# Performance work log

Hardware: AMD Instinct MI355X
Metric: run time of the kernel (lower is better)

Reference implementation:

```python
import jax, jax.numpy as jnp
import numpy as np

BATCH = 262144
CLUSTER = 100

def _boost_generators():
    # Standard Lorentz boost generators K_x, K_y, K_z (symmetric, metric (+,-,-,-)).
    K = np.zeros((3, 4, 4), dtype=np.float32)
    for j in range(3):
        K[j, 0, j + 1] = 1.0
        K[j, j + 1, 0] = 1.0
    return jnp.asarray(K)

def setup_inputs() -> dict:
    key = jax.random.key(0)
    k1, k2, k3, k4 = jax.random.split(key, 4)
    T = jax.random.normal(k1, (BATCH, CLUSTER, 4), dtype=jnp.float32)
    # build() initializes boosts/bias uniform[0,1) scaled by 0.33 (|b| < 1 => gamma real)
    Bo = jax.random.uniform(k2, (CLUSTER, 3), dtype=jnp.float32) * 0.33
    Bi = jax.random.uniform(k3, (1, 3), dtype=jnp.float32) * 0.33
    W = jax.random.uniform(k4, (CLUSTER, 1), dtype=jnp.float32)
    K_mats = _boost_generators()
    return {"T": T, "Bo": Bo, "Bi": Bi, "W": W, "K_mats": K_mats}

def _lorentz(x, boosts, K_mats, weights=None):
    # x: (batch, C, 4), boosts: (C, 3) -> (batch, 4)
    mag = jnp.sqrt(jnp.sum(boosts * boosts, axis=1, keepdims=True))  # (C,1)
    n = boosts / mag                                                  # (C,3)
    g = 1.0 / jnp.sqrt(1.0 - mag * mag)                               # (C,1) gamma
    nK = jnp.einsum('cj,jad->cad', n, K_mats)                         # (C,4,4)
    nK2 = jnp.einsum('cab,cbd->cad', nK, nK)                          # (C,4,4)
    B = (jnp.eye(4, dtype=x.dtype)[None]
         - (g * mag)[..., None] * nK
         + (g - 1.0)[..., None] * nK2)                                # (C,4,4)
    if weights is not None:
        B = weights[:, :, None] * B                                   # per-element scalar weight
    # sum over cluster of B_c @ x[:, c]
    return jnp.einsum('cad,bcd->ba', B, x)

def reference(T, Bo, Bi, W, K_mats):
    summed = _lorentz(T, Bo, K_mats, weights=W)            # (batch, 4)
    out = _lorentz(summed[:, None, :], Bi, K_mats)         # (batch, 4)
    return out.reshape(T.shape[0], 1, 4)
```

## Files before the change

### kernel.cpp

```cpp
#include <hip/hip_runtime.h>
#include <math.h>

#define BATCH   262144
#define CLUSTER 100

__device__ inline void boost_mat(float bx, float by, float bz, float B[4][4]) {
    float m2  = bx * bx + by * by + bz * bz;
    float mag = sqrtf(m2);
    float nx = bx / mag, ny = by / mag, nz = bz / mag;
    float g  = 1.0f / sqrtf(1.0f - mag * mag);
    float gm = g * mag;
    float gm1 = g - 1.0f;
    float n[3] = {nx, ny, nz};
    B[0][0] = 1.0f + gm1 * (nx * nx + ny * ny + nz * nz);
    for (int j = 0; j < 3; ++j) {
        B[0][j + 1] = -gm * n[j];
        B[j + 1][0] = -gm * n[j];
    }
    for (int i = 0; i < 3; ++i)
        for (int j = 0; j < 3; ++j)
            B[i + 1][j + 1] = ((i == j) ? 1.0f : 0.0f) + gm1 * n[i] * n[j];
}

#define DOT4(mm, vv) ((mm).x*(vv).x + (mm).y*(vv).y + (mm).z*(vv).z + (mm).w*(vv).w)

__global__ __launch_bounds__(256) void lorentz_fused_kernel(
        const float* __restrict__ T,
        const float* __restrict__ Bo,
        const float* __restrict__ Bi,
        const float* __restrict__ W,
        float* __restrict__ out) {
    __shared__ float sM[CLUSTER * 16];

    int tid = threadIdx.x;
    if (tid < CLUSTER) {
        float BiM[4][4], BoM[4][4];
        boost_mat(Bi[0], Bi[1], Bi[2], BiM);
        boost_mat(Bo[tid * 3 + 0], Bo[tid * 3 + 1], Bo[tid * 3 + 2], BoM);
        float w = W[tid];
        for (int a = 0; a < 4; ++a)
            for (int d = 0; d < 4; ++d) {
                float s = 0.0f;
                for (int e = 0; e < 4; ++e)
                    s += BiM[a][e] * (w * BoM[e][d]);
                sM[tid * 16 + a * 4 + d] = s;
            }
    }
    __syncthreads();

    int wave = tid >> 6;
    int lane = tid & 63;
    int q = lane & 7;
    int g = lane >> 3;
    long long base = (long long)blockIdx.x * 64 + wave * 16;
    long long row0 = base + g;
    long long row1 = base + g + 8;

    const float* P0 = T + row0 * (CLUSTER * 4);
    const float* P1 = T + row1 * (CLUSTER * 4);

    float4 a0 = {0.f, 0.f, 0.f, 0.f};
    float4 a1 = a0;

    #pragma unroll 4
    for (int t = 0; t < 12; ++t) {
        int c = 8 * t + q;
        float4 v0 = *(const float4*)(P0 + c * 4);
        float4 v1 = *(const float4*)(P1 + c * 4);
        const float4* m = (const float4*)(sM + c * 16);
        float4 m0 = m[0], m1 = m[1], m2 = m[2], m3 = m[3];
        a0.x += DOT4(m0, v0); a0.y += DOT4(m1, v0); a0.z += DOT4(m2, v0); a0.w += DOT4(m3, v0);
        a1.x += DOT4(m0, v1); a1.y += DOT4(m1, v1); a1.z += DOT4(m2, v1); a1.w += DOT4(m3, v1);
    }
    if (q < 4) {
        int c = 96 + q;
        float4 v0 = *(const float4*)(P0 + c * 4);
        float4 v1 = *(const float4*)(P1 + c * 4);
        const float4* m = (const float4*)(sM + c * 16);
        float4 m0 = m[0], m1 = m[1], m2 = m[2], m3 = m[3];
        a0.x += DOT4(m0, v0); a0.y += DOT4(m1, v0); a0.z += DOT4(m2, v0); a0.w += DOT4(m3, v0);
        a1.x += DOT4(m0, v1); a1.y += DOT4(m1, v1); a1.z += DOT4(m2, v1); a1.w += DOT4(m3, v1);
    }

    #define RED(f) f += __shfl_xor(f, 1); f += __shfl_xor(f, 2); f += __shfl_xor(f, 4);
    RED(a0.x) RED(a0.y) RED(a0.z) RED(a0.w)
    RED(a1.x) RED(a1.y) RED(a1.z) RED(a1.w)
    #undef RED

    if (q == 0) ((float4*)out)[row0] = a0;
    if (q == 1) ((float4*)out)[row1] = a1;
}

extern "C" void kernel_launch(void* const* d_in, const int* in_sizes, int n_in,
                              void* d_out, int out_size, void* d_ws, size_t ws_size,
                              hipStream_t stream) {
    const float* T  = (const float*)d_in[0];
    const float* Bo = (const float*)d_in[1];
    const float* Bi = (const float*)d_in[2];
    const float* W  = (const float*)d_in[3];

    float* out = (float*)d_out;

    int blocks = BATCH / 64;
    lorentz_fused_kernel<<<blocks, 256, 0, stream>>>(T, Bo, Bi, W, out);
}
```

Before: 77.82 us.

## Prefetch T before matrix setup and widen lane layout to four rows per thread

Issues the first global loads of T before the per-block boost-matrix computation and barrier, so memory latency overlaps the setup work. Each thread now handles four rows, with sixteen lanes per row instead of eight, and the next iteration's loads are software-pipelined. The shared matrix is stored in a row-split layout to change the LDS access pattern. This adds one extra shuffle stage in the reduction and uses more registers, which may reduce occupancy.

```diff
diff --git a/kernel.cpp b/kernel.cpp
--- a/kernel.cpp
+++ b/kernel.cpp
@@ -30,9 +30,25 @@
         const float* __restrict__ Bi,
         const float* __restrict__ W,
         float* __restrict__ out) {
-    __shared__ float sM[CLUSTER * 16];
+    __shared__ float sMr[4][CLUSTER * 4];
 
-    int tid = threadIdx.x;
+    int tid  = threadIdx.x;
+    int wave = tid >> 6;
+    int lane = tid & 63;
+    int q = lane & 15;
+    int g = lane >> 4;
+    long long base = (long long)blockIdx.x * 64 + wave * 16;
+
+    const float* P0 = T + (base + g +  0) * (CLUSTER * 4);
+    const float* P1 = T + (base + g +  4) * (CLUSTER * 4);
+    const float* P2 = T + (base + g +  8) * (CLUSTER * 4);
+    const float* P3 = T + (base + g + 12) * (CLUSTER * 4);
+
+    float4 v0 = *(const float4*)(P0 + q * 4);
+    float4 v1 = *(const float4*)(P1 + q * 4);
+    float4 v2 = *(const float4*)(P2 + q * 4);
+    float4 v3 = *(const float4*)(P3 + q * 4);
+
     if (tid < CLUSTER) {
         float BiM[4][4], BoM[4][4];
         boost_mat(Bi[0], Bi[1], Bi[2], BiM);
@@ -43,52 +59,62 @@
                 float s = 0.0f;
                 for (int e = 0; e < 4; ++e)
                     s += BiM[a][e] * (w * BoM[e][d]);
-                sM[tid * 16 + a * 4 + d] = s;
+                sMr[a][tid * 4 + d] = s;
             }
     }
     __syncthreads();
 
-    int wave = tid >> 6;
-    int lane = tid & 63;
-    int q = lane & 7;
-    int g = lane >> 3;
-    long long base = (long long)blockIdx.x * 64 + wave * 16;
-    long long row0 = base + g;
-    long long row1 = base + g + 8;
+    float4 a0 = {0.f, 0.f, 0.f, 0.f};
+    float4 a1 = a0, a2 = a0, a3 = a0;
 
-    const float* P0 = T + row0 * (CLUSTER * 4);
-    const float* P1 = T + row1 * (CLUSTER * 4);
+    #define ACCSTEP(c)                                                        \
+    {                                                                         \
+        float4 m0 = *(const float4*)&sMr[0][(c) * 4];                         \
+        float4 m1 = *(const float4*)&sMr[1][(c) * 4];                         \
+        float4 m2 = *(const float4*)&sMr[2][(c) * 4];                         \
+        float4 m3 = *(const float4*)&sMr[3][(c) * 4];                         \
+        a0.x += DOT4(m0, v0); a0.y += DOT4(m1, v0); a0.z += DOT4(m2, v0); a0.w += DOT4(m3, v0); \
+        a1.x += DOT4(m0, v1); a1.y += DOT4(m1, v1); a1.z += DOT4(m2, v1); a1.w += DOT4(m3, v1); \
+        a2.x += DOT4(m0, v2); a2.y += DOT4(m1, v2); a2.z += DOT4(m2, v2); a2.w += DOT4(m3, v2); \
+        a3.x += DOT4(m0, v3); a3.y += DOT4(m1, v3); a3.z += DOT4(m2, v3); a3.w += DOT4(m3, v3); \
+    }
 
-    float4 a0 = {0.f, 0.f, 0.f, 0.f};
-    float4 a1 = a0;
-
-    #pragma unroll 4
-    for (int t = 0; t < 12; ++t) {
-        int c = 8 * t + q;
-        float4 v0 = *(const float4*)(P0 + c * 4);
-        float4 v1 = *(const float4*)(P1 + c * 4);
-        const float4* m = (const float4*)(sM + c * 16);
-        float4 m0 = m[0], m1 = m[1], m2 = m[2], m3 = m[3];
-        a0.x += DOT4(m0, v0); a0.y += DOT4(m1, v0); a0.z += DOT4(m2, v0); a0.w += DOT4(m3, v0);
-        a1.x += DOT4(m0, v1); a1.y += DOT4(m1, v1); a1.z += DOT4(m2, v1); a1.w += DOT4(m3, v1);
+    for (int t = 0; t < 6; ++t) {
+        int c = 16 * t + q;
+        ACCSTEP(c)
+        if (t < 5) {
+            int cn = c + 16;
+            v0 = *(const float4*)(P0 + cn * 4);
+            v1 = *(const float4*)(P1 + cn * 4);
+            v2 = *(const float4*)(P2 + cn * 4);
+            v3 = *(const float4*)(P3 + cn * 4);
+        } else if (q < 4) {
+            int cn = 96 + q;
+            v0 = *(const float4*)(P0 + cn * 4);
+            v1 = *(const float4*)(P1 + cn * 4);
+            v2 = *(const float4*)(P2 + cn * 4);
+            v3 = *(const float4*)(P3 + cn * 4);
+        }
     }
     if (q < 4) {
-        int c = 96 + q;
-        float4 v0 = *(const float4*)(P0 + c * 4);
-        float4 v1 = *(const float4*)(P1 + c * 4);
-        const float4* m = (const float4*)(sM + c * 16);
-        float4 m0 = m[0], m1 = m[1], m2 = m[2], m3 = m[3];
-        a0.x += DOT4(m0, v0); a0.y += DOT4(m1, v0); a0.z += DOT4(m2, v0); a0.w += DOT4(m3, v0);
-        a1.x += DOT4(m0, v1); a1.y += DOT4(m1, v1); a1.z += DOT4(m2, v1); a1.w += DOT4(m3, v1);
+        ACCSTEP(96 + q)
     }
+    #undef ACCSTEP
 
-    #define RED(f) f += __shfl_xor(f, 1); f += __shfl_xor(f, 2); f += __shfl_xor(f, 4);
+    #define RED(f) f += __shfl_xor(f, 1); f += __shfl_xor(f, 2); \
+                   f += __shfl_xor(f, 4); f += __shfl_xor(f, 8);
     RED(a0.x) RED(a0.y) RED(a0.z) RED(a0.w)
     RED(a1.x) RED(a1.y) RED(a1.z) RED(a1.w)
+    RED(a2.x) RED(a2.y) RED(a2.z) RED(a2.w)
+    RED(a3.x) RED(a3.y) RED(a3.z) RED(a3.w)
     #undef RED
 
-    if (q == 0) ((float4*)out)[row0] = a0;
-    if (q == 1) ((float4*)out)[row1] = a1;
+    float4 o = a0;
+    if (q == 1) o = a1;
+    if (q == 2) o = a2;
+    if (q == 3) o = a3;
+    if (q < 4)
+        ((float4*)out)[base + g + 4 * q] = o;
 }
 
 extern "C" void kernel_launch(void* const* d_in, const int* in_sizes, int n_in,
```

New measurement: 82.90 us. 1.07x slower.

## Process multiple row tiles per block to amortize matrix setup

Applied to the files above, without the earlier changes.

Each block now loops over four 64-row tiles, so the per-block setup (computing the 100 combined boost matrices and the barrier) runs once per 256 rows instead of once per 64. The shared matrix storage is also changed from per-cluster 4x4 blocks to row-major planes, which alters the LDS access pattern for the float4 loads. The grid becomes four times smaller (1024 blocks), which reduces parallelism available to hide memory latency on a bandwidth-bound kernel.

```diff
diff --git a/kernel.cpp b/kernel.cpp
--- a/kernel.cpp
+++ b/kernel.cpp
@@ -3,6 +3,7 @@
 
 #define BATCH   262144
 #define CLUSTER 100
+#define TILES   4
 
 __device__ inline void boost_mat(float bx, float by, float bz, float B[4][4]) {
     float m2  = bx * bx + by * by + bz * bz;
@@ -24,83 +25,90 @@
 
 #define DOT4(mm, vv) ((mm).x*(vv).x + (mm).y*(vv).y + (mm).z*(vv).z + (mm).w*(vv).w)
 
-__global__ __launch_bounds__(256) void lorentz_fused_kernel(
-        const float* __restrict__ T,
-        const float* __restrict__ Bo,
-        const float* __restrict__ Bi,
-        const float* __restrict__ W,
-        float* __restrict__ out) {
-    __shared__ float sM[CLUSTER * 16];
+__global__ __launch_bounds__(256) void lorentz_multitile_kernel(
+        const float4* __restrict__ T4,
+        const float*  __restrict__ Bo,
+        const float*  __restrict__ Bi,
+        const float*  __restrict__ W,
+        float4* __restrict__ out4) {
+    __shared__ float sMr[4][CLUSTER * 4];
 
-    int tid = threadIdx.x;
+    int tid  = threadIdx.x;
+    int w    = tid >> 6;
+    int lane = tid & 63;
+    int q = lane & 7;
+    int g = lane >> 3;
+
     if (tid < CLUSTER) {
         float BiM[4][4], BoM[4][4];
         boost_mat(Bi[0], Bi[1], Bi[2], BiM);
         boost_mat(Bo[tid * 3 + 0], Bo[tid * 3 + 1], Bo[tid * 3 + 2], BoM);
-        float w = W[tid];
+        float wt = W[tid];
         for (int a = 0; a < 4; ++a)
             for (int d = 0; d < 4; ++d) {
                 float s = 0.0f;
                 for (int e = 0; e < 4; ++e)
-                    s += BiM[a][e] * (w * BoM[e][d]);
-                sM[tid * 16 + a * 4 + d] = s;
+                    s += BiM[a][e] * (wt * BoM[e][d]);
+                sMr[a][tid * 4 + d] = s;
             }
     }
     __syncthreads();
 
-    int wave = tid >> 6;
-    int lane = tid & 63;
-    int q = lane & 7;
-    int g = lane >> 3;
-    long long base = (long long)blockIdx.x * 64 + wave * 16;
-    long long row0 = base + g;
-    long long row1 = base + g + 8;
+    long long blockRow = (long long)blockIdx.x * (64 * TILES);
 
-    const float* P0 = T + row0 * (CLUSTER * 4);
-    const float* P1 = T + row1 * (CLUSTER * 4);
+    #pragma unroll 1
+    for (int tile = 0; tile < TILES; ++tile) {
+        long long base = blockRow + tile * 64 + w * 16;
+        const float4* P0 = T4 + (base + g)     * CLUSTER;
+        const float4* P1 = T4 + (base + g + 8) * CLUSTER;
 
-    float4 a0 = {0.f, 0.f, 0.f, 0.f};
-    float4 a1 = a0;
+        float4 a0 = {0.f, 0.f, 0.f, 0.f};
+        float4 a1 = a0;
 
-    #pragma unroll 4
-    for (int t = 0; t < 12; ++t) {
-        int c = 8 * t + q;
-        float4 v0 = *(const float4*)(P0 + c * 4);
-        float4 v1 = *(const float4*)(P1 + c * 4);
-        const float4* m = (const float4*)(sM + c * 16);
-        float4 m0 = m[0], m1 = m[1], m2 = m[2], m3 = m[3];
-        a0.x += DOT4(m0, v0); a0.y += DOT4(m1, v0); a0.z += DOT4(m2, v0); a0.w += DOT4(m3, v0);
-        a1.x += DOT4(m0, v1); a1.y += DOT4(m1, v1); a1.z += DOT4(m2, v1); a1.w += DOT4(m3, v1);
+        #pragma unroll 4
+        for (int t = 0; t < 12; ++t) {
+            int c = 8 * t + q;
+            float4 v0 = P0[c];
+            float4 v1 = P1[c];
+            float4 m0 = *(const float4*)&sMr[0][c * 4];
+            float4 m1 = *(const float4*)&sMr[1][c * 4];
+            float4 m2 = *(const float4*)&sMr[2][c * 4];
+            float4 m3 = *(const float4*)&sMr[3][c * 4];
+            a0.x += DOT4(m0, v0); a0.y += DOT4(m1, v0); a0.z += DOT4(m2, v0); a0.w += DOT4(m3, v0);
+            a1.x += DOT4(m0, v1); a1.y += DOT4(m1, v1); a1.z += DOT4(m2, v1); a1.w += DOT4(m3, v1);
+        }
+        if (q < 4) {
+            int c = 96 + q;
+            float4 v0 = P0[c];
+            float4 v1 = P1[c];
+            float4 m0 = *(const float4*)&sMr[0][c * 4];
+            float4 m1 = *(const float4*)&sMr[1][c * 4];
+            float4 m2 = *(const float4*)&sMr[2][c * 4];
+            float4 m3 = *(const float4*)&sMr[3][c * 4];
+            a0.x += DOT4(m0, v0); a0.y += DOT4(m1, v0); a0.z += DOT4(m2, v0); a0.w += DOT4(m3, v0);
+            a1.x += DOT4(m0, v1); a1.y += DOT4(m1, v1); a1.z += DOT4(m2, v1); a1.w += DOT4(m3, v1);
+        }
+
+        #define RED(f) f += __shfl_xor(f, 1); f += __shfl_xor(f, 2); f += __shfl_xor(f, 4);
+        RED(a0.x) RED(a0.y) RED(a0.z) RED(a0.w)
+        RED(a1.x) RED(a1.y) RED(a1.z) RED(a1.w)
+        #undef RED
+
+        if (q == 0) out4[base + g]     = a0;
+        if (q == 1) out4[base + g + 8] = a1;
     }
-    if (q < 4) {
-        int c = 96 + q;
-        float4 v0 = *(const float4*)(P0 + c * 4);
-        float4 v1 = *(const float4*)(P1 + c * 4);
-        const float4* m = (const float4*)(sM + c * 16);
-        float4 m0 = m[0], m1 = m[1], m2 = m[2], m3 = m[3];
-        a0.x += DOT4(m0, v0); a0.y += DOT4(m1, v0); a0.z += DOT4(m2, v0); a0.w += DOT4(m3, v0);
-        a1.x += DOT4(m0, v1); a1.y += DOT4(m1, v1); a1.z += DOT4(m2, v1); a1.w += DOT4(m3, v1);
-    }
-
-    #define RED(f) f += __shfl_xor(f, 1); f += __shfl_xor(f, 2); f += __shfl_xor(f, 4);
-    RED(a0.x) RED(a0.y) RED(a0.z) RED(a0.w)
-    RED(a1.x) RED(a1.y) RED(a1.z) RED(a1.w)
-    #undef RED
-
-    if (q == 0) ((float4*)out)[row0] = a0;
-    if (q == 1) ((float4*)out)[row1] = a1;
 }
 
 extern "C" void kernel_launch(void* const* d_in, const int* in_sizes, int n_in,
                               void* d_out, int out_size, void* d_ws, size_t ws_size,
                               hipStream_t stream) {
-    const float* T  = (const float*)d_in[0];
-    const float* Bo = (const float*)d_in[1];
-    const float* Bi = (const float*)d_in[2];
-    const float* W  = (const float*)d_in[3];
+    const float4* T4 = (const float4*)d_in[0];
+    const float*  Bo = (const float*)d_in[1];
+    const float*  Bi = (const float*)d_in[2];
+    const float*  W  = (const float*)d_in[3];
 
-    float* out = (float*)d_out;
+    float4* out4 = (float4*)d_out;
 
-    int blocks = BATCH / 64;
-    lorentz_fused_kernel<<<blocks, 256, 0, stream>>>(T, Bo, Bi, W, out);
+    int blocks = BATCH / (64 * TILES);
+    lorentz_multitile_kernel<<<blocks, 256, 0, stream>>>(T4, Bo, Bi, W, out4);
 }
```

Result: slower. 80.50 us (+3.4%).
